# Kernel tuning notes

Measured on AMD Instinct MI355X. Metric: run time of the kernel, lower is better.

Reference implementation:

```python
import jax, jax.numpy as jnp
import numpy as np

NEG = -1e9  # large negative for masked logits (TRT uses dtype min)

def _rotate_every_two(x):
    # pairs (x0,x1) -> (-x1, x0), interleaved along last dim
    xr = x.reshape(*x.shape[:-1], -1, 2)
    rot = jnp.stack([-xr[..., 1], xr[..., 0]], axis=-1)
    return rot.reshape(x.shape)

def _apply_rope(x, cos, sin):
    # rot_dim == cos.shape[-1]; here it equals the full inner dim
    rot_dim = cos.shape[-1]
    x_rot, x_pass = x[..., :rot_dim], x[..., rot_dim:]
    x_rot = x_rot * cos + _rotate_every_two(x_rot) * sin
    return jnp.concatenate([x_rot, x_pass], axis=-1) if x_pass.shape[-1] else x_rot

def setup_inputs() -> dict:
    key = jax.random.key(0)
    ks = jax.random.split(key, 12)
    B, N, D_MODEL, H, DH = 2, 2048, 1024, 16, 64
    INNER = H * DH
    x = jax.random.normal(ks[0], (B, N, D_MODEL), dtype=jnp.float32)
    # rope angles: build realistic cos/sin tables repeated per head
    pos = jnp.arange(N, dtype=jnp.float32)
    inv = 1.0 / (10000.0 ** (jnp.arange(0, DH, 2, dtype=jnp.float32) / DH))
    ang = pos[:, None] * inv[None, :]              # [N, DH/2]
    ang = jnp.repeat(ang, 2, axis=-1)              # [N, DH] interleaved pairs
    ang = jnp.tile(ang, (1, H))                    # [N, INNER]
    rope_cos = jnp.broadcast_to(jnp.cos(ang)[None], (B, N, INNER)).astype(jnp.float32)
    rope_sin = jnp.broadcast_to(jnp.sin(ang)[None], (B, N, INNER)).astype(jnp.float32)
    input_lengths = jax.random.randint(ks[1], (B,), N // 2, N + 1, dtype=jnp.int32)
    s = 1.0 / np.sqrt(D_MODEL)
    Wq = jax.random.normal(ks[2], (D_MODEL, INNER), dtype=jnp.float32) * s
    bq = jnp.zeros((INNER,), jnp.float32)
    Wk = jax.random.normal(ks[3], (D_MODEL, INNER), dtype=jnp.float32) * s
    bk = jnp.zeros((INNER,), jnp.float32)
    Wv = jax.random.normal(ks[4], (D_MODEL, INNER), dtype=jnp.float32) * s
    bv = jnp.zeros((INNER,), jnp.float32)
    Wo = jax.random.normal(ks[5], (INNER, D_MODEL), dtype=jnp.float32) * (1.0 / np.sqrt(INNER))
    bo = jnp.zeros((D_MODEL,), jnp.float32)
    return {"x": x, "rope_cos": rope_cos, "rope_sin": rope_sin,
            "input_lengths": input_lengths,
            "Wq": Wq, "bq": bq, "Wk": Wk, "bk": bk, "Wv": Wv, "bv": bv,
            "Wo": Wo, "bo": bo}

def reference(x, rope_cos, rope_sin, input_lengths, Wq, bq, Wk, bk, Wv, bv, Wo, bo):
    B, N, _ = x.shape
    H, DH = 16, 64
    q = x @ Wq + bq
    k = x @ Wk + bk
    v = x @ Wv + bv
    q = _apply_rope(q, rope_cos, rope_sin)
    k = _apply_rope(k, rope_cos, rope_sin)
    # split heads: [B,N,H,DH] -> [B,H,N,DH]
    q = q.reshape(B, N, H, DH).transpose(0, 2, 1, 3)
    k = k.reshape(B, N, H, DH).transpose(0, 2, 1, 3)
    v = v.reshape(B, N, H, DH).transpose(0, 2, 1, 3)
    # NOTE: faithful to the non-plugin source path, q is NOT pre-scaled
    scores = jnp.einsum('bhqd,bhkd->bhqk', q, k)
    key_mask = jnp.arange(N)[None, :] < input_lengths[:, None]  # [B,N]
    scores = scores + jnp.where(key_mask, 0.0, NEG).astype(scores.dtype)[:, None, None, :]
    probs = jax.nn.softmax(scores, axis=-1)
    ctx = jnp.einsum('bhqk,bhkd->bhqd', probs, v)  # [B,H,N,DH]
    ctx = ctx.transpose(0, 2, 1, 3).reshape(B, N, H * DH)
    out = ctx @ Wo + bo
    out = out * key_mask[..., None].astype(out.dtype)
    return out
```

## Files before the change

### kernel.cpp

```cpp
#include <hip/hip_runtime.h>
#include <hip/hip_bf16.h>


typedef __fp16 fp16x2 __attribute__((ext_vector_type(2)));
typedef _Float16 f16x8 __attribute__((ext_vector_type(8)));
typedef float f32x4 __attribute__((ext_vector_type(4)));
typedef float f32x16 __attribute__((ext_vector_type(16)));

#define NEGBIG (-1.0e9f)

__device__ inline f32x4 mfma16(f16x8 a, f16x8 b, f32x4 c) {
  return __builtin_amdgcn_mfma_f32_16x16x32_f16(a, b, c, 0, 0, 0);
}
__device__ inline f32x16 mfma32(f16x8 a, f16x8 b, f32x16 c) {
  return __builtin_amdgcn_mfma_f32_32x32x16_f16(a, b, c, 0, 0, 0);
}

__device__ inline void gload16(const void* g, void* l) {
  __builtin_amdgcn_global_load_lds(
      (const __attribute__((address_space(1))) void*)g,
      (__attribute__((address_space(3))) void*)l, 16, 0, 0);
}

__device__ inline unsigned pk2u(float a, float b) {
  union { fp16x2 h; unsigned u; } x;
  x.h = __builtin_amdgcn_cvt_pkrtz(a, b);
  return x.u;
}

__global__ __launch_bounds__(256) void prep_kernel(
    const float* __restrict__ x, const float* __restrict__ Wq,
    const float* __restrict__ Wk, const float* __restrict__ Wv,
    const float* __restrict__ Wo, _Float16* __restrict__ xh,
    _Float16* __restrict__ wt) {
  __shared__ float tile[32][33];
  const int z = blockIdx.z;
  const int tx = threadIdx.x, ty = threadIdx.y;
  if (z == 4) {
    const int bid = blockIdx.y * 32 + blockIdx.x;
    const int t = ty * 32 + tx;
#pragma unroll
    for (int i = 0; i < 4; ++i) {
      const int o = bid * 1024 + i * 256 + t;
      const float4 v = ((const float4*)x)[o];
      union { _Float16 h[4]; short4 s; } u;
      u.h[0] = (_Float16)v.x; u.h[1] = (_Float16)v.y;
      u.h[2] = (_Float16)v.z; u.h[3] = (_Float16)v.w;
      ((short4*)xh)[o] = u.s;
    }
    return;
  }
  const float* W = (z == 0) ? Wq : (z == 1) ? Wk : (z == 2) ? Wv : Wo;
  _Float16* dh = wt + (size_t)z * 1024 * 1024;
  const int j0 = blockIdx.x * 32, k0 = blockIdx.y * 32;
  for (int i = ty; i < 32; i += 8)
    tile[i][tx] = W[(size_t)(k0 + i) * 1024 + j0 + tx];
  __syncthreads();
  for (int i = ty; i < 32; i += 8)
    dh[(size_t)(j0 + i) * 1024 + k0 + tx] = (_Float16)tile[tx][i];
}

template <int TM, int EPI>
__global__ __launch_bounds__(256) void gemm_kernel(
    const _Float16* __restrict__ A, const _Float16* __restrict__ B,
    const float* __restrict__ bias0, const float* __restrict__ bias1,
    const float* __restrict__ bias2,
    const float* __restrict__ ropeC, const float* __restrict__ ropeS,
    const int* __restrict__ lens,
    _Float16* __restrict__ outQK, _Float16* __restrict__ outVT,
    float* __restrict__ outF) {
  constexpr int MI = TM / 32;
  __shared__ __align__(16) _Float16 smem[(TM + 128) * 32];
  const int t = threadIdx.x;
  const int w = t >> 6, lane = t & 63;
  const int wr = w >> 1, wc = w & 1;
  const int fr = lane & 15, fg = lane >> 4;
  const int mtile = blockIdx.x, ntile = blockIdx.y;

  const int srow = t >> 2;
  const int skel = (t & 3) << 3;
  const size_t aBase = (size_t)(mtile * TM + srow) * 1024 + skel;
  const size_t bBase = (size_t)(ntile * 128 + srow) * 1024 + skel;
  const int ldst = t * 8;
  _Float16* lA = &smem[0];
  _Float16* lB = &smem[TM * 32];

  f32x4 acc[MI][4];
#pragma unroll
  for (int i = 0; i < MI; ++i)
#pragma unroll
    for (int j = 0; j < 4; ++j) {
      acc[i][j][0] = 0.f; acc[i][j][1] = 0.f; acc[i][j][2] = 0.f; acc[i][j][3] = 0.f;
    }

  for (int k0 = 0; k0 < 1024; k0 += 32) {
    gload16(A + aBase + k0, lA + ldst);
    if constexpr (TM == 128) gload16(A + aBase + k0 + 64 * 1024, lA + ldst + 2048);
    gload16(B + bBase + k0, lB + ldst);
    gload16(B + bBase + k0 + 64 * 1024, lB + ldst + 2048);
    __syncthreads();

    f16x8 af[MI], bf[4];
#pragma unroll
    for (int mi = 0; mi < MI; ++mi)
      af[mi] = *(const f16x8*)&lA[(wr * (TM / 2) + mi * 16 + fr) * 32 + fg * 8];
#pragma unroll
    for (int ni = 0; ni < 4; ++ni)
      bf[ni] = *(const f16x8*)&lB[(wc * 64 + ni * 16 + fr) * 32 + fg * 8];
#pragma unroll
    for (int mi = 0; mi < MI; ++mi)
#pragma unroll
      for (int ni = 0; ni < 4; ++ni)
        acc[mi][ni] = mfma16(af[mi], bf[ni], acc[mi][ni]);
    __syncthreads();
  }

  const int rowbase = mtile * TM + wr * (TM / 2);
  const int colbase = ntile * 128 + wc * 64;

  if constexpr (EPI == 0) {
    const int which = colbase >> 10;
    if (which < 2) {
      const float* bias = which ? bias1 : bias0;
#pragma unroll
      for (int ni = 0; ni < 4; ++ni) {
        const int gcol = colbase + ni * 16 + fr;
        const int jj = gcol & 1023;
        const int hh = jj >> 6, dd = jj & 63;
        const float bv = bias[jj];
#pragma unroll
        for (int mi = 0; mi < MI; ++mi) {
#pragma unroll
          for (int r = 0; r < 4; ++r) {
            const int grow = rowbase + mi * 16 + fg * 4 + r;
            const int b = grow >> 11, n = grow & 2047;
            float val = acc[mi][ni][r] + bv;
            float part = __shfl_xor(val, 1);
            const size_t ro = (size_t)(b * 2048 + n) * 1024 + jj;
            const float c = ropeC[ro], s = ropeS[ro];
            float rot = (fr & 1) ? (val * c + part * s) : (val * c - part * s);
            if (!which) rot *= 1.44269504f;
            outQK[((size_t)((which * 2 + b) * 16 + hh) * 2048 + n) * 64 + dd] =
                (_Float16)rot;
          }
        }
      }
    } else {
#pragma unroll
      for (int ni = 0; ni < 4; ++ni) {
        const int gcol = colbase + ni * 16 + fr;
        const int jj = gcol & 1023;
        const int hh = jj >> 6, dd = jj & 63;
        const float bv = bias2[jj];
#pragma unroll
        for (int mi = 0; mi < MI; ++mi) {
          const int n0 = rowbase + mi * 16 + fg * 4;
          const int b = n0 >> 11, n = n0 & 2047;
          union { _Float16 h[4]; short4 s4; } u;
#pragma unroll
          for (int r = 0; r < 4; ++r) u.h[r] = (_Float16)(acc[mi][ni][r] + bv);
          *(short4*)(outVT + ((size_t)(b * 16 + hh) * 64 + dd) * 2048 + n) = u.s4;
        }
      }
    }
  } else {
    const int b = rowbase >> 11;
    const int len = lens[b];
#pragma unroll
    for (int ni = 0; ni < 4; ++ni) {
      const int gcol = colbase + ni * 16 + fr;
      const float bv = bias0[gcol];
#pragma unroll
      for (int mi = 0; mi < MI; ++mi) {
#pragma unroll
        for (int r = 0; r < 4; ++r) {
          const int m = rowbase + mi * 16 + fg * 4 + r;
          const int n = m & 2047;
          float val = acc[mi][ni][r] + bv;
          if (n >= len) val = 0.f;
          outF[(size_t)m * 1024 + gcol] = val;
        }
      }
    }
  }
}

__global__ __launch_bounds__(128, 2) void attn_kernel(
    const _Float16* __restrict__ qk, const _Float16* __restrict__ vt,
    const int* __restrict__ lens, _Float16* __restrict__ ctx) {
  __shared__ __align__(16) char lds[32768];
  const int t = threadIdx.x;
  const int w = t >> 6, lane = t & 63;
  const int lq = lane & 31, hi = lane >> 5;
  const int fid = blockIdx.x;
  const int qtile = (fid >> 3) & 31;
  const int bh = (fid & 7) + ((fid >> 8) << 3);
  const int b = bh >> 4, h = bh & 15;
  const int len = lens[b];
  const int q0w = qtile * 64 + w * 32;
  const size_t qoff = (size_t)(b * 16 + h) * 2048 * 64;
  const size_t koff = (size_t)((2 + b) * 16 + h) * 2048 * 64;
  const size_t voff = (size_t)(b * 16 + h) * 64 * 2048;

  f16x8 qf[4];
#pragma unroll
  for (int ks = 0; ks < 4; ++ks)
    qf[ks] = *(const f16x8*)(qk + qoff + (size_t)(q0w + lq) * 64 + ks * 16 + hi * 8);

  const int srow = t >> 3;
  const int sslot = (t & 7) ^ (srow & 7);
  const size_t kg = koff + (size_t)srow * 64 + sslot * 8;
  const size_t vg = voff + (size_t)srow * 2048 + sslot * 8;

  f32x16 o0, o1;
#pragma unroll
  for (int i = 0; i < 16; ++i) { o0[i] = 0.f; o1[i] = 0.f; }
  float mrun = -1e30f, lsum = 0.f;

#define STAGE(bi, k0_) do { \
    char* dst = lds + (bi) * 16384 + t * 16; \
    const _Float16* ks_ = qk + kg + (size_t)(k0_) * 64; \
    const _Float16* vs_ = vt + vg + (k0_); \
    gload16(ks_, dst); gload16(ks_ + 1024, dst + 2048); \
    gload16(ks_ + 2048, dst + 4096); gload16(ks_ + 3072, dst + 6144); \
    gload16(vs_, dst + 8192); gload16(vs_ + 32768, dst + 10240); \
    gload16(vs_ + 65536, dst + 12288); gload16(vs_ + 98304, dst + 14336); \
  } while (0)

  const int nkb = (len + 63) >> 6;
  STAGE(0, 0);

  for (int kb = 0; kb < nkb; ++kb) {
    const int cur = kb & 1;
    if (kb + 1 < nkb) {
      STAGE(cur ^ 1, (kb + 1) * 64);
      asm volatile("s_waitcnt vmcnt(8)" ::: "memory");
    } else {
      asm volatile("s_waitcnt vmcnt(0)" ::: "memory");
    }
    __builtin_amdgcn_s_barrier();

    const char* Kb = lds + cur * 16384;
    const char* Vb = Kb + 8192;
    const int rsw = (lq & 7) << 4;

    f32x16 s0, s1;
#pragma unroll
    for (int i = 0; i < 16; ++i) { s0[i] = 0.f; s1[i] = 0.f; }
    __builtin_amdgcn_s_setprio(1);
#pragma unroll
    for (int ks = 0; ks < 4; ++ks) {
      const int col = ks * 32 + hi * 16;
      const f16x8 k0f = *(const f16x8*)(Kb + lq * 128 + (col ^ rsw));
      const f16x8 k1f = *(const f16x8*)(Kb + (32 + lq) * 128 + (col ^ rsw));
      s0 = mfma32(k0f, qf[ks], s0);
      s1 = mfma32(k1f, qf[ks], s1);
    }
    __builtin_amdgcn_s_setprio(0);

    if (kb == nkb - 1 && (len & 63)) {
#pragma unroll
      for (int r = 0; r < 16; ++r) {
        const int key = kb * 64 + (r & 3) + ((r >> 2) << 3) + hi * 4;
        if (key >= len) s0[r] = NEGBIG;
        if (key + 32 >= len) s1[r] = NEGBIG;
      }
    }

    float mx = s0[0];
#pragma unroll
    for (int r = 1; r < 16; ++r) mx = fmaxf(mx, s0[r]);
#pragma unroll
    for (int r = 0; r < 16; ++r) mx = fmaxf(mx, s1[r]);
    mx = fmaxf(mx, __shfl_xor(mx, 32));

    if (!__all(mx <= mrun + 8.f)) {
      const float mnew = fmaxf(mrun, mx);
      const float scq = exp2f(mrun - mnew);
      mrun = mnew;
      lsum *= scq;
      float sc[16];
#pragma unroll
      for (int r = 0; r < 16; ++r)
        sc[r] = __shfl(scq, (r & 3) + ((r >> 2) << 3) + hi * 4);
#pragma unroll
      for (int r = 0; r < 16; ++r) { o0[r] *= sc[r]; o1[r] *= sc[r]; }
    }

    unsigned W[16];
    float ps = 0.f;
#pragma unroll
    for (int u = 0; u < 4; ++u) {
      const float p0 = exp2f(s0[4 * u + 0] - mrun);
      const float p1 = exp2f(s0[4 * u + 1] - mrun);
      const float p2 = exp2f(s0[4 * u + 2] - mrun);
      const float p3 = exp2f(s0[4 * u + 3] - mrun);
      ps += (p0 + p1) + (p2 + p3);
      W[2 * u] = pk2u(p0, p1);
      W[2 * u + 1] = pk2u(p2, p3);
    }
#pragma unroll
    for (int u = 0; u < 4; ++u) {
      const float p0 = exp2f(s1[4 * u + 0] - mrun);
      const float p1 = exp2f(s1[4 * u + 1] - mrun);
      const float p2 = exp2f(s1[4 * u + 2] - mrun);
      const float p3 = exp2f(s1[4 * u + 3] - mrun);
      ps += (p0 + p1) + (p2 + p3);
      W[8 + 2 * u] = pk2u(p0, p1);
      W[8 + 2 * u + 1] = pk2u(p2, p3);
    }
    ps += __shfl_xor(ps, 32);
    lsum += ps;

    __builtin_amdgcn_s_setprio(1);
#pragma unroll
    for (int ks = 0; ks < 4; ++ks) {
      const unsigned w0 = W[4 * ks + 0], w1 = W[4 * ks + 1];
      const unsigned w2 = W[4 * ks + 2], w3 = W[4 * ks + 3];
      const unsigned sendA = hi ? w0 : w2;
      const unsigned sendB = hi ? w1 : w3;
      const unsigned recvA = __shfl_xor(sendA, 32);
      const unsigned recvB = __shfl_xor(sendB, 32);
      union { unsigned u[4]; f16x8 v; } af;
      af.u[0] = hi ? recvA : w0;
      af.u[1] = hi ? recvB : w1;
      af.u[2] = hi ? w2 : recvA;
      af.u[3] = hi ? w3 : recvB;
      const int col = ks * 32 + hi * 16;
      const f16x8 v0f = *(const f16x8*)(Vb + lq * 128 + (col ^ rsw));
      const f16x8 v1f = *(const f16x8*)(Vb + (32 + lq) * 128 + (col ^ rsw));
      o0 = mfma32(af.v, v0f, o0);
      o1 = mfma32(af.v, v1f, o1);
    }
    __builtin_amdgcn_s_setprio(0);

    asm volatile("" ::: "memory");
    __builtin_amdgcn_s_barrier();
  }
#undef STAGE

  const float li = 1.f / lsum;
#pragma unroll
  for (int r = 0; r < 16; ++r) {
    const int qr = (r & 3) + ((r >> 2) << 3) + hi * 4;
    const float lr = __shfl(li, qr);
    const int n = q0w + qr;
    _Float16* dst = ctx + (size_t)(b * 2048 + n) * 1024 + h * 64;
    dst[lq] = (_Float16)(o0[r] * lr);
    dst[32 + lq] = (_Float16)(o1[r] * lr);
  }
}


extern "C" void kernel_launch(void* const* d_in, const int* in_sizes, int n_in,
                              void* d_out, int out_size, void* d_ws, size_t ws_size,
                              hipStream_t stream) {
  const float* x = (const float*)d_in[0];
  const float* rc = (const float*)d_in[1];
  const float* rs = (const float*)d_in[2];
  const int* lens = (const int*)d_in[3];
  const float* Wq = (const float*)d_in[4];
  const float* bq = (const float*)d_in[5];
  const float* Wk = (const float*)d_in[6];
  const float* bk = (const float*)d_in[7];
  const float* Wv = (const float*)d_in[8];
  const float* bv = (const float*)d_in[9];
  const float* Wo = (const float*)d_in[10];
  const float* bo = (const float*)d_in[11];
  float* out = (float*)d_out;

  char* ws = (char*)d_ws;
  const size_t MB = 1024 * 1024;
  _Float16* XH = (_Float16*)(ws + 0);
  _Float16* WT = (_Float16*)(ws + 8 * MB);
  _Float16* QK = (_Float16*)(ws + 16 * MB);
  _Float16* VT = (_Float16*)(ws + 32 * MB);
  _Float16* CTX = (_Float16*)(ws + 40 * MB);

  prep_kernel<<<dim3(32, 32, 5), dim3(32, 8), 0, stream>>>(x, Wq, Wk, Wv, Wo,
                                                           XH, WT);
  gemm_kernel<128, 0><<<dim3(32, 24), 256, 0, stream>>>(
      XH, WT, bq, bk, bv, rc, rs, nullptr, QK, VT, nullptr);
  attn_kernel<<<1024, 128, 0, stream>>>(QK, VT, lens, CTX);
  gemm_kernel<64, 2><<<dim3(64, 8), 256, 0, stream>>>(
      CTX, WT + (size_t)3 * 1024 * 1024, bo, nullptr, nullptr, nullptr,
      nullptr, lens, nullptr, nullptr, out);
}
```

Baseline: 169.6 us.

## Split attention over two key segments and merge partials in a combine kernel

The attention kernel now splits each (batch, head, q-tile) over two halves of the key range (flash-decoding style split-K), doubling grid size to 2048 blocks. Key tiles shrink from 64 to 32, which halves LDS so occupancy can rise to 4 blocks per CU. Each block writes unnormalized fp32 partial outputs plus the running max and sum, and a new combine kernel rescales and merges the two halves into fp16 context. In exchange it adds an extra launch, fp32 partial traffic of about 32MB, and more loop iterations with fewer MFMAs per barrier.

```diff
diff --git a/kernel.cpp b/kernel.cpp
--- a/kernel.cpp
+++ b/kernel.cpp
@@ -185,16 +185,18 @@
   }
 }
 
-__global__ __launch_bounds__(128, 2) void attn_kernel(
+__global__ __launch_bounds__(128, 4) void attn_kernel(
     const _Float16* __restrict__ qk, const _Float16* __restrict__ vt,
-    const int* __restrict__ lens, _Float16* __restrict__ ctx) {
-  __shared__ __align__(16) char lds[32768];
+    const int* __restrict__ lens, float* __restrict__ po,
+    float2* __restrict__ ml) {
+  __shared__ __align__(16) char lds[16384];
   const int t = threadIdx.x;
   const int w = t >> 6, lane = t & 63;
   const int lq = lane & 31, hi = lane >> 5;
-  const int fid = blockIdx.x;
-  const int qtile = (fid >> 3) & 31;
-  const int bh = (fid & 7) + ((fid >> 8) << 3);
+  const int gid = blockIdx.x;
+  const int bh_seg = (gid & 7) + ((gid >> 8) << 3);
+  const int qtile = (gid >> 3) & 31;
+  const int bh = bh_seg >> 1, seg = bh_seg & 1;
   const int b = bh >> 4, h = bh & 15;
   const int len = lens[b];
   const int q0w = qtile * 64 + w * 32;
@@ -208,70 +210,69 @@
     qf[ks] = *(const f16x8*)(qk + qoff + (size_t)(q0w + lq) * 64 + ks * 16 + hi * 8);
 
   const int srow = t >> 3;
-  const int sslot = (t & 7) ^ (srow & 7);
-  const size_t kg = koff + (size_t)srow * 64 + sslot * 8;
-  const size_t vg = voff + (size_t)srow * 2048 + sslot * 8;
+  const int ss = (t & 7) ^ (srow & 7);
+  const size_t kg = koff + (size_t)srow * 64 + ss * 8;
+  const int vd = srow + ((ss >> 2) << 5);
+  const size_t vg1 = voff + (size_t)vd * 2048 + (ss & 3) * 8;
+  const size_t vg2 = voff + (size_t)(vd + 16) * 2048 + (ss & 3) * 8;
 
   f32x16 o0, o1;
 #pragma unroll
   for (int i = 0; i < 16; ++i) { o0[i] = 0.f; o1[i] = 0.f; }
   float mrun = -1e30f, lsum = 0.f;
 
-#define STAGE(bi, k0_) do { \
-    char* dst = lds + (bi) * 16384 + t * 16; \
-    const _Float16* ks_ = qk + kg + (size_t)(k0_) * 64; \
-    const _Float16* vs_ = vt + vg + (k0_); \
-    gload16(ks_, dst); gload16(ks_ + 1024, dst + 2048); \
-    gload16(ks_ + 2048, dst + 4096); gload16(ks_ + 3072, dst + 6144); \
-    gload16(vs_, dst + 8192); gload16(vs_ + 32768, dst + 10240); \
-    gload16(vs_ + 65536, dst + 12288); gload16(vs_ + 98304, dst + 14336); \
+#define STAGE(bi, kb_) do { \
+    char* dst = lds + (bi) * 8192 + t * 16; \
+    const size_t k064 = (size_t)(kb_) * 2048;  \
+    gload16(qk + kg + k064, dst); \
+    gload16(qk + kg + k064 + 1024, dst + 2048); \
+    gload16(vt + vg1 + (kb_) * 32, dst + 4096); \
+    gload16(vt + vg2 + (kb_) * 32, dst + 6144); \
   } while (0)
 
-  const int nkb = (len + 63) >> 6;
-  STAGE(0, 0);
-
-  for (int kb = 0; kb < nkb; ++kb) {
-    const int cur = kb & 1;
-    if (kb + 1 < nkb) {
-      STAGE(cur ^ 1, (kb + 1) * 64);
-      asm volatile("s_waitcnt vmcnt(8)" ::: "memory");
+  const int nkb = (len + 31) >> 5;
+  const int nk0 = (nkb + 1) >> 1;
+  const int tb0 = seg ? nk0 : 0;
+  const int tb1 = seg ? nkb : nk0;
+
+  STAGE(0, tb0);
+
+  for (int kb = tb0; kb < tb1; ++kb) {
+    const int cur = (kb - tb0) & 1;
+    if (kb + 1 < tb1) {
+      STAGE(cur ^ 1, kb + 1);
+      asm volatile("s_waitcnt vmcnt(4)" ::: "memory");
     } else {
       asm volatile("s_waitcnt vmcnt(0)" ::: "memory");
     }
     __builtin_amdgcn_s_barrier();
 
-    const char* Kb = lds + cur * 16384;
-    const char* Vb = Kb + 8192;
+    const char* Kb = lds + cur * 8192;
+    const char* Vb = Kb + 4096;
     const int rsw = (lq & 7) << 4;
 
-    f32x16 s0, s1;
-#pragma unroll
-    for (int i = 0; i < 16; ++i) { s0[i] = 0.f; s1[i] = 0.f; }
+    f32x16 s0;
+#pragma unroll
+    for (int i = 0; i < 16; ++i) s0[i] = 0.f;
     __builtin_amdgcn_s_setprio(1);
 #pragma unroll
     for (int ks = 0; ks < 4; ++ks) {
-      const int col = ks * 32 + hi * 16;
-      const f16x8 k0f = *(const f16x8*)(Kb + lq * 128 + (col ^ rsw));
-      const f16x8 k1f = *(const f16x8*)(Kb + (32 + lq) * 128 + (col ^ rsw));
-      s0 = mfma32(k0f, qf[ks], s0);
-      s1 = mfma32(k1f, qf[ks], s1);
+      const f16x8 kf = *(const f16x8*)(Kb + lq * 128 + ((ks * 32 + hi * 16) ^ rsw));
+      s0 = mfma32(kf, qf[ks], s0);
     }
     __builtin_amdgcn_s_setprio(0);
 
-    if (kb == nkb - 1 && (len & 63)) {
+    if (kb == nkb - 1 && (len & 31)) {
 #pragma unroll
       for (int r = 0; r < 16; ++r) {
-        const int key = kb * 64 + (r & 3) + ((r >> 2) << 3) + hi * 4;
+        const int key = kb * 32 + (r & 3) + ((r >> 2) << 3) + hi * 4;
         if (key >= len) s0[r] = NEGBIG;
-        if (key + 32 >= len) s1[r] = NEGBIG;
       }
     }
 
     float mx = s0[0];
 #pragma unroll
     for (int r = 1; r < 16; ++r) mx = fmaxf(mx, s0[r]);
-#pragma unroll
-    for (int r = 0; r < 16; ++r) mx = fmaxf(mx, s1[r]);
     mx = fmaxf(mx, __shfl_xor(mx, 32));
 
     if (!__all(mx <= mrun + 8.f)) {
@@ -287,7 +288,7 @@
       for (int r = 0; r < 16; ++r) { o0[r] *= sc[r]; o1[r] *= sc[r]; }
     }
 
-    unsigned W[16];
+    unsigned W[8];
     float ps = 0.f;
 #pragma unroll
     for (int u = 0; u < 4; ++u) {
@@ -299,22 +300,12 @@
       W[2 * u] = pk2u(p0, p1);
       W[2 * u + 1] = pk2u(p2, p3);
     }
-#pragma unroll
-    for (int u = 0; u < 4; ++u) {
-      const float p0 = exp2f(s1[4 * u + 0] - mrun);
-      const float p1 = exp2f(s1[4 * u + 1] - mrun);
-      const float p2 = exp2f(s1[4 * u + 2] - mrun);
-      const float p3 = exp2f(s1[4 * u + 3] - mrun);
-      ps += (p0 + p1) + (p2 + p3);
-      W[8 + 2 * u] = pk2u(p0, p1);
-      W[8 + 2 * u + 1] = pk2u(p2, p3);
-    }
     ps += __shfl_xor(ps, 32);
     lsum += ps;
 
     __builtin_amdgcn_s_setprio(1);
 #pragma unroll
-    for (int ks = 0; ks < 4; ++ks) {
+    for (int ks = 0; ks < 2; ++ks) {
       const unsigned w0 = W[4 * ks + 0], w1 = W[4 * ks + 1];
       const unsigned w2 = W[4 * ks + 2], w3 = W[4 * ks + 3];
       const unsigned sendA = hi ? w0 : w2;
@@ -326,9 +317,9 @@
       af.u[1] = hi ? recvB : w1;
       af.u[2] = hi ? w2 : recvA;
       af.u[3] = hi ? w3 : recvB;
-      const int col = ks * 32 + hi * 16;
-      const f16x8 v0f = *(const f16x8*)(Vb + lq * 128 + (col ^ rsw));
-      const f16x8 v1f = *(const f16x8*)(Vb + (32 + lq) * 128 + (col ^ rsw));
+      const int g0 = ks * 2 + hi;
+      const f16x8 v0f = *(const f16x8*)(Vb + lq * 128 + ((g0 << 4) ^ rsw));
+      const f16x8 v1f = *(const f16x8*)(Vb + lq * 128 + (((g0 + 4) << 4) ^ rsw));
       o0 = mfma32(af.v, v0f, o0);
       o1 = mfma32(af.v, v1f, o1);
     }
@@ -339,15 +330,43 @@
   }
 #undef STAGE
 
-  const float li = 1.f / lsum;
+  const size_t rowbase = (size_t)bh * 2048 + q0w;
+  float* pod = po + ((size_t)seg * 65536 + rowbase) * 64;
 #pragma unroll
   for (int r = 0; r < 16; ++r) {
     const int qr = (r & 3) + ((r >> 2) << 3) + hi * 4;
-    const float lr = __shfl(li, qr);
-    const int n = q0w + qr;
-    _Float16* dst = ctx + (size_t)(b * 2048 + n) * 1024 + h * 64;
-    dst[lq] = (_Float16)(o0[r] * lr);
-    dst[32 + lq] = (_Float16)(o1[r] * lr);
+    pod[qr * 64 + lq] = o0[r];
+    pod[qr * 64 + 32 + lq] = o1[r];
+  }
+  if (hi == 0) {
+    float2 v; v.x = mrun; v.y = lsum;
+    ml[(size_t)seg * 65536 + rowbase + lq] = v;
+  }
+}
+
+__global__ __launch_bounds__(256) void combine_kernel(
+    const float* __restrict__ po, const float2* __restrict__ ml,
+    _Float16* __restrict__ ctx) {
+  const int tid = blockIdx.x * 256 + threadIdx.x;
+  const int row = tid >> 2, dg = tid & 3;
+  const float2 a = ml[row], c = ml[65536 + row];
+  const float m = fmaxf(a.x, c.x);
+  const float e0 = exp2f(a.x - m), e1 = exp2f(c.x - m);
+  const float inv = 1.f / (a.y * e0 + c.y * e1);
+  const float f0 = e0 * inv, f1 = e1 * inv;
+  const float4* p0 = (const float4*)(po + (size_t)row * 64 + dg * 16);
+  const float4* p1 = (const float4*)(po + (size_t)(65536 + row) * 64 + dg * 16);
+  const int bh = row >> 11, n = row & 2047, b = bh >> 4, h = bh & 15;
+  _Float16* dst = ctx + ((size_t)(b * 2048 + n) * 1024 + h * 64 + dg * 16);
+#pragma unroll
+  for (int i = 0; i < 4; ++i) {
+    const float4 v0 = p0[i], v1 = p1[i];
+    union { _Float16 h[4]; short4 s4; } u;
+    u.h[0] = (_Float16)(v0.x * f0 + v1.x * f1);
+    u.h[1] = (_Float16)(v0.y * f0 + v1.y * f1);
+    u.h[2] = (_Float16)(v0.z * f0 + v1.z * f1);
+    u.h[3] = (_Float16)(v0.w * f0 + v1.w * f1);
+    *(short4*)(dst + i * 4) = u.s4;
   }
 }
 
@@ -376,12 +395,15 @@
   _Float16* QK = (_Float16*)(ws + 16 * MB);
   _Float16* VT = (_Float16*)(ws + 32 * MB);
   _Float16* CTX = (_Float16*)(ws + 40 * MB);
+  float* PO = (float*)(ws + 48 * MB);
+  float2* ML = (float2*)(ws + 81 * MB);
 
   prep_kernel<<<dim3(32, 32, 5), dim3(32, 8), 0, stream>>>(x, Wq, Wk, Wv, Wo,
                                                            XH, WT);
   gemm_kernel<128, 0><<<dim3(32, 24), 256, 0, stream>>>(
       XH, WT, bq, bk, bv, rc, rs, nullptr, QK, VT, nullptr);
-  attn_kernel<<<1024, 128, 0, stream>>>(QK, VT, lens, CTX);
+  attn_kernel<<<2048, 128, 0, stream>>>(QK, VT, lens, PO, ML);
+  combine_kernel<<<1024, 256, 0, stream>>>(PO, ML, CTX);
   gemm_kernel<64, 2><<<dim3(64, 8), 256, 0, stream>>>(
       CTX, WT + (size_t)3 * 1024 * 1024, bo, nullptr, nullptr, nullptr,
       nullptr, lens, nullptr, nullptr, out);
```

Result: faster. 161.2 us (-4.9%).
